# Optimization experiments

Measured on AMD Instinct MI355X. Metric: run time of the kernel, lower is better.

Reference implementation:

```python
import jax, jax.numpy as jnp
import numpy as np

TAU = 0.1
MASK_VAL = 1e9


def setup_inputs() -> dict:
    key = jax.random.key(0)
    ka, kb = jax.random.split(key)
    B, D = 4096, 512
    return {
        "view_a": jax.random.normal(ka, (B, D), dtype=jnp.float32),
        "view_b": jax.random.normal(kb, (B, D), dtype=jnp.float32),
    }


def _l2norm(x):
    return x / jnp.maximum(jnp.linalg.norm(x, axis=-1, keepdims=True), 1e-12)


def reference(view_a, view_b):
    a = _l2norm(view_a)
    b = _l2norm(view_b)
    B = a.shape[0]
    labels = jnp.arange(B)  # start_i = 0 (single device)
    mask = jnp.eye(B, dtype=a.dtype) * MASK_VAL

    logits_aa = a @ a.T / TAU - mask
    logits_bb = b @ b.T / TAU - mask
    logits_ab = a @ b.T / TAU
    logits_ba = b @ a.T / TAU

    full_a = jnp.concatenate([logits_ab, logits_aa], axis=1)  # [B, 2B]
    full_b = jnp.concatenate([logits_ba, logits_bb], axis=1)

    def ce(logits):
        logp = jax.nn.log_softmax(logits, axis=-1)
        return -jnp.mean(jnp.take_along_axis(logp, labels[:, None], axis=-1))

    loss = (ce(full_a) + ce(full_b)) / 2

    pred = jnp.argmax(full_a, axis=-1)
    acc = 100.0 * jnp.sum(pred == labels) / B
    return loss, acc
```

## Files before the change

kernel.cpp:

```cpp
#include <hip/hip_runtime.h>
#include <stdint.h>


#define BN 4096
#define DK 512
#define NSPLIT 16
#define NEG_BIG -1e30f
#define SCL 0.15625f
#define SCL2 0.225396744f
#define C2 14.4269504f
#define TILE_BYTES (64 * DK)

typedef __attribute__((ext_vector_type(16))) float floatx16;
typedef __attribute__((ext_vector_type(8))) int intx8;

__global__ void __launch_bounds__(256) prep_kernel(
    const float* __restrict__ A, const float* __restrict__ Bv,
    unsigned char* __restrict__ An, unsigned char* __restrict__ Bn,
    float* __restrict__ diag, float* __restrict__ out) {
  if (blockIdx.x == 0 && threadIdx.x < 2) out[threadIdx.x] = 0.0f;
  const int w = threadIdx.x >> 6, lane = threadIdx.x & 63;
  const int row = blockIdx.x * 4 + w;
  const float4* pa4 = (const float4*)(A + (size_t)row * DK);
  const float4* pb4 = (const float4*)(Bv + (size_t)row * DK);
  float4 a0 = pa4[lane * 2], a1 = pa4[lane * 2 + 1];
  float4 b0 = pb4[lane * 2], b1 = pb4[lane * 2 + 1];
  float ssa = a0.x * a0.x + a0.y * a0.y + a0.z * a0.z + a0.w * a0.w +
              a1.x * a1.x + a1.y * a1.y + a1.z * a1.z + a1.w * a1.w;
  float ssb = b0.x * b0.x + b0.y * b0.y + b0.z * b0.z + b0.w * b0.w +
              b1.x * b1.x + b1.y * b1.y + b1.z * b1.z + b1.w * b1.w;
  float sab = a0.x * b0.x + a0.y * b0.y + a0.z * b0.z + a0.w * b0.w +
              a1.x * b1.x + a1.y * b1.y + a1.z * b1.z + a1.w * b1.w;
#pragma unroll
  for (int off = 32; off > 0; off >>= 1) {
    ssa += __shfl_xor(ssa, off);
    ssb += __shfl_xor(ssb, off);
    sab += __shfl_xor(sab, off);
  }
  float na = fmaxf(sqrtf(ssa), 1e-12f);
  float nb = fmaxf(sqrtf(ssb), 1e-12f);
  const float s = 8.0f;
  float sa = s / na, sb = s / nb;
  const int doff = (lane >> 2) * 32 + (lane & 1) * 16 + ((lane >> 1) & 1) * 8;
  {
    int v0 = __builtin_amdgcn_cvt_pk_fp8_f32(a0.x * sa, a0.y * sa, 0, false);
    v0 = __builtin_amdgcn_cvt_pk_fp8_f32(a0.z * sa, a0.w * sa, v0, true);
    int v1 = __builtin_amdgcn_cvt_pk_fp8_f32(a1.x * sa, a1.y * sa, 0, false);
    v1 = __builtin_amdgcn_cvt_pk_fp8_f32(a1.z * sa, a1.w * sa, v1, true);
    int2 pv; pv.x = v0; pv.y = v1;
    *(int2*)(An + (size_t)row * DK + doff) = pv;
  }
  {
    int v0 = __builtin_amdgcn_cvt_pk_fp8_f32(b0.x * sb, b0.y * sb, 0, false);
    v0 = __builtin_amdgcn_cvt_pk_fp8_f32(b0.z * sb, b0.w * sb, v0, true);
    int v1 = __builtin_amdgcn_cvt_pk_fp8_f32(b1.x * sb, b1.y * sb, 0, false);
    v1 = __builtin_amdgcn_cvt_pk_fp8_f32(b1.z * sb, b1.w * sb, v1, true);
    int2 pv; pv.x = v0; pv.y = v1;
    *(int2*)(Bn + (size_t)row * DK + doff) = pv;
  }
  if (lane == 0) diag[row] = (sab / (na * nb)) * 10.0f;
}

__global__ void __launch_bounds__(256, 2) tiles_kernel(
    const unsigned char* __restrict__ An, const unsigned char* __restrict__ Bn,
    float* __restrict__ pSA, float* __restrict__ pMA, float* __restrict__ pSB) {
  __shared__ __align__(16) unsigned char smem[2 * TILE_BYTES];

  const int rb = blockIdx.x;
  const int split = blockIdx.y;
  const int tid = threadIdx.x;
  const int lane = tid & 63, w = tid >> 6;
  const int n5 = lane & 31, h = lane >> 5;
  const int r0 = rb * 128;
  const int myrow = r0 + w * 32 + n5;

  intx8 aw[8];
  auto loadfrags = [&](const unsigned char* base) {
    const unsigned char* p = base + (size_t)myrow * DK + h * 16;
#pragma unroll
    for (int i = 0; i < 8; ++i) {
      int4 c0 = *(const int4*)(p + i * 64);
      int4 c1 = *(const int4*)(p + i * 64 + 32);
      intx8 v = {c0.x, c0.y, c0.z, c0.w, c1.x, c1.y, c1.z, c1.w};
      aw[i] = v;
    }
  };

  float l[16], mx[16];
#pragma unroll
  for (int r = 0; r < 16; ++r) { l[r] = 0.f; mx[r] = NEG_BIG; }

  auto stage = [&](unsigned char* buf, int jt) {
    const unsigned char* csrc = (jt < 64) ? An : Bn;
    const int cb = (jt & 63) * 64;
#pragma unroll
    for (int ii = 0; ii < 8; ++ii) {
      const int cp = w * 8 + ii;
      const int cl = cp * 2 + h;
      const unsigned char* src =
          csrc + (size_t)(cb + cl) * DK + ((n5 ^ (cl & 31)) * 16);
      __builtin_amdgcn_global_load_lds(
          (const __attribute__((address_space(1))) void*)src,
          (__attribute__((address_space(3))) void*)(buf + cp * 1024),
          16, 0, 0);
    }
  };

  stage(smem, split * 8);
  loadfrags(An);
  __syncthreads();

  for (int u = 0; u < 16; ++u) {
    const int t = u & 7;
    const int jt = split * 8 + t;
    unsigned char* cur = smem + (u & 1) * TILE_BYTES;
    unsigned char* nxt = smem + ((u + 1) & 1) * TILE_BYTES;
    if (u < 15) stage(nxt, split * 8 + ((t + 1) & 7));

    floatx16 acc[2];
#pragma unroll
    for (int cs = 0; cs < 2; ++cs)
#pragma unroll
      for (int r = 0; r < 16; ++r) acc[cs][r] = 0.f;

    const unsigned char* bbase = cur + (size_t)n5 * DK;
#pragma unroll
    for (int i = 0; i < 8; ++i) {
      const int p1 = ((4 * i + h) ^ n5) * 16;
      const int p2 = ((4 * i + 2 + h) ^ n5) * 16;
#pragma unroll
      for (int cs = 0; cs < 2; ++cs) {
        int4 b0 = *(const int4*)(bbase + cs * 32 * DK + p1);
        int4 b1 = *(const int4*)(bbase + cs * 32 * DK + p2);
        intx8 bw = {b0.x, b0.y, b0.z, b0.w, b1.x, b1.y, b1.z, b1.w};
        acc[cs] = __builtin_amdgcn_mfma_scale_f32_32x32x64_f8f6f4(
            aw[i], bw, acc[cs], 0, 0, 0, 0x7F7F7F7F, 0, 0x7F7F7F7F);
      }
    }

    const bool dtile = (((jt & 63) >> 1) == rb);
    const int colbase = (jt & 63) * 64;
    const bool passA = (u < 8);
#pragma unroll
    for (int r = 0; r < 16; ++r) {
      float v0 = acc[0][r], v1 = acc[1][r];
      if (dtile) {
        const int rowg = r0 + w * 32 + (r & 3) + 8 * (r >> 2) + 4 * h;
        if (rowg == colbase + n5)      v0 = NEG_BIG;
        if (rowg == colbase + 32 + n5) v1 = NEG_BIG;
      }
      if (passA) mx[r] = fmaxf(mx[r], fmaxf(v0, v1));
      l[r] += exp2f(fmaf(v0, SCL2, -C2)) + exp2f(fmaf(v1, SCL2, -C2));
    }

    if (u == 7) {
#pragma unroll
      for (int off = 1; off < 32; off <<= 1)
#pragma unroll
        for (int r = 0; r < 16; ++r) {
          l[r] += __shfl_xor(l[r], off);
          mx[r] = fmaxf(mx[r], __shfl_xor(mx[r], off));
        }
      if (n5 == 0) {
#pragma unroll
        for (int r = 0; r < 16; ++r) {
          const int row = r0 + w * 32 + (r & 3) + 8 * (r >> 2) + 4 * h;
          pSA[split * BN + row] = l[r];
          pMA[split * BN + row] = mx[r] * SCL;
        }
      }
#pragma unroll
      for (int r = 0; r < 16; ++r) l[r] = 0.f;
      loadfrags(Bn);
    }
    __syncthreads();
  }

#pragma unroll
  for (int off = 1; off < 32; off <<= 1)
#pragma unroll
    for (int r = 0; r < 16; ++r) l[r] += __shfl_xor(l[r], off);
  if (n5 == 0) {
#pragma unroll
    for (int r = 0; r < 16; ++r) {
      const int row = r0 + w * 32 + (r & 3) + 8 * (r >> 2) + 4 * h;
      pSB[split * BN + row] = l[r];
    }
  }
}

__global__ void __launch_bounds__(256) finalize_kernel(
    const float* __restrict__ pSA, const float* __restrict__ pMA,
    const float* __restrict__ pSB, const float* __restrict__ diag,
    float* __restrict__ out) {
  const int row = blockIdx.x * 256 + threadIdx.x;
  float SA = 0.f, SB = 0.f, MA = NEG_BIG;
#pragma unroll
  for (int s = 0; s < NSPLIT; ++s) {
    SA += pSA[s * BN + row];
    SB += pSB[s * BN + row];
    MA = fmaxf(MA, pMA[s * BN + row]);
  }
  const float d = diag[row];
  const float eL = exp2f(fmaf(d, 1.44269504f, -C2));
  float lseA = 10.0f + logf(SA + eL);
  float lseB = 10.0f + logf(SB + eL);
  float lossi = (lseA - d) + (lseB - d);
  float corr = (d >= MA) ? 1.f : 0.f;
#pragma unroll
  for (int off = 32; off > 0; off >>= 1) {
    lossi += __shfl_xor(lossi, off);
    corr += __shfl_xor(corr, off);
  }
  __shared__ float sred[2][4];
  if ((threadIdx.x & 63) == 0) {
    int w = threadIdx.x >> 6;
    sred[0][w] = lossi; sred[1][w] = corr;
  }
  __syncthreads();
  if (threadIdx.x == 0) {
    float ls = sred[0][0] + sred[0][1] + sred[0][2] + sred[0][3];
    float cs = sred[1][0] + sred[1][1] + sred[1][2] + sred[1][3];
    atomicAdd(&out[0], ls * (1.0f / 8192.0f));
    atomicAdd(&out[1], cs * (100.0f / 4096.0f));
  }
}

extern "C" void kernel_launch(void* const* d_in, const int* in_sizes, int n_in,
                              void* d_out, int out_size, void* d_ws, size_t ws_size,
                              hipStream_t stream) {
  const float* A = (const float*)d_in[0];
  const float* Bv = (const float*)d_in[1];
  unsigned char* An = (unsigned char*)d_ws;
  unsigned char* Bn = An + (size_t)BN * DK;
  float* diag = (float*)(Bn + (size_t)BN * DK);
  float* pSA = diag + BN;
  float* pMA = pSA + NSPLIT * BN;
  float* pSB = pMA + NSPLIT * BN;
  float* out = (float*)d_out;

  prep_kernel<<<BN / 4, 256, 0, stream>>>(A, Bv, An, Bn, diag, out);
  tiles_kernel<<<dim3(32, 16), 256, 0, stream>>>(An, Bn, pSA, pMA, pSB);
  finalize_kernel<<<BN / 256, 256, 0, stream>>>(pSA, pMA, pSB, diag, out);
}
```

Baseline: 121.9 us.

## Exploit Gram matrix symmetry: compute upper-triangle tiles only with row and column partial sums

Stacks A and B into a single 8192-row fp8 matrix and computes only the upper-triangular 128x64 tiles of its Gram matrix, one tile per block across 4160 blocks. Each tile contributes both row and column exp-sums (and maxes for the argmax), so the matmul work is roughly halved compared with computing A·[A;B]^T and B·[B;A]^T separately. In exchange, partial buffers grow to hundreds of slices that prep has to zero-fill and finalize has to reduce serially. Blocks are also much shorter, each loading a fresh A fragment with no double buffering, which adds launch and load overhead and reduces latency hiding.

```diff
diff --git a/kernel.cpp b/kernel.cpp
--- a/kernel.cpp
+++ b/kernel.cpp
@@ -4,21 +4,28 @@
 
 #define BN 4096
 #define DK 512
-#define NSPLIT 16
 #define NEG_BIG -1e30f
 #define SCL 0.15625f
 #define SCL2 0.225396744f
 #define C2 14.4269504f
 #define TILE_BYTES (64 * DK)
+#define NBLK 4160
 
 typedef __attribute__((ext_vector_type(16))) float floatx16;
 typedef __attribute__((ext_vector_type(8))) int intx8;
 
 __global__ void __launch_bounds__(256) prep_kernel(
     const float* __restrict__ A, const float* __restrict__ Bv,
-    unsigned char* __restrict__ An, unsigned char* __restrict__ Bn,
-    float* __restrict__ diag, float* __restrict__ out) {
-  if (blockIdx.x == 0 && threadIdx.x < 2) out[threadIdx.x] = 0.0f;
+    unsigned char* __restrict__ Gn, float* __restrict__ diag,
+    float* __restrict__ out, float* __restrict__ zbase,
+    float* __restrict__ mbase) {
+  const int gtid = blockIdx.x * 256 + threadIdx.x;
+  if (gtid < 2) out[gtid] = 0.0f;
+  for (int idx = gtid; idx < (128 + 64) * 8192; idx += 1024 * 256)
+    zbase[idx] = 0.0f;
+  for (int idx = gtid; idx < (128 + 32) * 4096; idx += 1024 * 256)
+    mbase[idx] = NEG_BIG;
+
   const int w = threadIdx.x >> 6, lane = threadIdx.x & 63;
   const int row = blockIdx.x * 4 + w;
   const float4* pa4 = (const float4*)(A + (size_t)row * DK);
@@ -48,7 +55,7 @@
     int v1 = __builtin_amdgcn_cvt_pk_fp8_f32(a1.x * sa, a1.y * sa, 0, false);
     v1 = __builtin_amdgcn_cvt_pk_fp8_f32(a1.z * sa, a1.w * sa, v1, true);
     int2 pv; pv.x = v0; pv.y = v1;
-    *(int2*)(An + (size_t)row * DK + doff) = pv;
+    *(int2*)(Gn + (size_t)row * DK + doff) = pv;
   }
   {
     int v0 = __builtin_amdgcn_cvt_pk_fp8_f32(b0.x * sb, b0.y * sb, 0, false);
@@ -56,27 +63,30 @@
     int v1 = __builtin_amdgcn_cvt_pk_fp8_f32(b1.x * sb, b1.y * sb, 0, false);
     v1 = __builtin_amdgcn_cvt_pk_fp8_f32(b1.z * sb, b1.w * sb, v1, true);
     int2 pv; pv.x = v0; pv.y = v1;
-    *(int2*)(Bn + (size_t)row * DK + doff) = pv;
+    *(int2*)(Gn + (size_t)(BN + row) * DK + doff) = pv;
   }
   if (lane == 0) diag[row] = (sab / (na * nb)) * 10.0f;
 }
 
 __global__ void __launch_bounds__(256, 2) tiles_kernel(
-    const unsigned char* __restrict__ An, const unsigned char* __restrict__ Bn,
-    float* __restrict__ pSA, float* __restrict__ pMA, float* __restrict__ pSB) {
-  __shared__ __align__(16) unsigned char smem[2 * TILE_BYTES];
-
-  const int rb = blockIdx.x;
-  const int split = blockIdx.y;
+    const unsigned char* __restrict__ Gn,
+    float* __restrict__ pRS, float* __restrict__ pCS,
+    float* __restrict__ pRM, float* __restrict__ pCM) {
+  __shared__ __align__(16) unsigned char smem[TILE_BYTES / 2 + 2048];
+
+  int bid = blockIdx.x, I = 0;
+  while (bid >= 128 - 2 * I) { bid -= 128 - 2 * I; ++I; }
+  const int j = 2 * I + bid;
+
   const int tid = threadIdx.x;
   const int lane = tid & 63, w = tid >> 6;
   const int n5 = lane & 31, h = lane >> 5;
-  const int r0 = rb * 128;
-  const int myrow = r0 + w * 32 + n5;
+  const int rbase = I * 128 + w * 32;
+  const int cbase = j * 64;
 
   intx8 aw[8];
-  auto loadfrags = [&](const unsigned char* base) {
-    const unsigned char* p = base + (size_t)myrow * DK + h * 16;
+  {
+    const unsigned char* p = Gn + (size_t)(rbase + n5) * DK + h * 16;
 #pragma unroll
     for (int i = 0; i < 8; ++i) {
       int4 c0 = *(const int4*)(p + i * 64);
@@ -84,124 +94,132 @@
       intx8 v = {c0.x, c0.y, c0.z, c0.w, c1.x, c1.y, c1.z, c1.w};
       aw[i] = v;
     }
-  };
-
-  float l[16], mx[16];
-#pragma unroll
-  for (int r = 0; r < 16; ++r) { l[r] = 0.f; mx[r] = NEG_BIG; }
-
-  auto stage = [&](unsigned char* buf, int jt) {
-    const unsigned char* csrc = (jt < 64) ? An : Bn;
-    const int cb = (jt & 63) * 64;
+  }
+
+  {
 #pragma unroll
     for (int ii = 0; ii < 8; ++ii) {
       const int cp = w * 8 + ii;
       const int cl = cp * 2 + h;
       const unsigned char* src =
-          csrc + (size_t)(cb + cl) * DK + ((n5 ^ (cl & 31)) * 16);
+          Gn + (size_t)(cbase + cl) * DK + ((n5 ^ (cl & 31)) * 16);
       __builtin_amdgcn_global_load_lds(
           (const __attribute__((address_space(1))) void*)src,
-          (__attribute__((address_space(3))) void*)(buf + cp * 1024),
+          (__attribute__((address_space(3))) void*)(smem + cp * 1024),
           16, 0, 0);
     }
-  };
-
-  stage(smem, split * 8);
-  loadfrags(An);
+  }
   __syncthreads();
 
-  for (int u = 0; u < 16; ++u) {
-    const int t = u & 7;
-    const int jt = split * 8 + t;
-    unsigned char* cur = smem + (u & 1) * TILE_BYTES;
-    unsigned char* nxt = smem + ((u + 1) & 1) * TILE_BYTES;
-    if (u < 15) stage(nxt, split * 8 + ((t + 1) & 7));
-
-    floatx16 acc[2];
-#pragma unroll
-    for (int cs = 0; cs < 2; ++cs)
-#pragma unroll
-      for (int r = 0; r < 16; ++r) acc[cs][r] = 0.f;
-
-    const unsigned char* bbase = cur + (size_t)n5 * DK;
-#pragma unroll
-    for (int i = 0; i < 8; ++i) {
-      const int p1 = ((4 * i + h) ^ n5) * 16;
-      const int p2 = ((4 * i + 2 + h) ^ n5) * 16;
-#pragma unroll
-      for (int cs = 0; cs < 2; ++cs) {
-        int4 b0 = *(const int4*)(bbase + cs * 32 * DK + p1);
-        int4 b1 = *(const int4*)(bbase + cs * 32 * DK + p2);
-        intx8 bw = {b0.x, b0.y, b0.z, b0.w, b1.x, b1.y, b1.z, b1.w};
-        acc[cs] = __builtin_amdgcn_mfma_scale_f32_32x32x64_f8f6f4(
-            aw[i], bw, acc[cs], 0, 0, 0, 0x7F7F7F7F, 0, 0x7F7F7F7F);
-      }
-    }
-
-    const bool dtile = (((jt & 63) >> 1) == rb);
-    const int colbase = (jt & 63) * 64;
-    const bool passA = (u < 8);
+  floatx16 acc[2];
+#pragma unroll
+  for (int cs = 0; cs < 2; ++cs)
+#pragma unroll
+    for (int r = 0; r < 16; ++r) acc[cs][r] = 0.f;
+
+  const unsigned char* bbase = smem + (size_t)n5 * DK;
+#pragma unroll
+  for (int i = 0; i < 8; ++i) {
+    const int p1 = ((4 * i + h) ^ n5) * 16;
+    const int p2 = ((4 * i + 2 + h) ^ n5) * 16;
+#pragma unroll
+    for (int cs = 0; cs < 2; ++cs) {
+      int4 b0 = *(const int4*)(bbase + cs * 32 * DK + p1);
+      int4 b1 = *(const int4*)(bbase + cs * 32 * DK + p2);
+      intx8 bw = {b0.x, b0.y, b0.z, b0.w, b1.x, b1.y, b1.z, b1.w};
+      acc[cs] = __builtin_amdgcn_mfma_scale_f32_32x32x64_f8f6f4(
+          aw[i], bw, acc[cs], 0, 0, 0, 0x7F7F7F7F, 0, 0x7F7F7F7F);
+    }
+  }
+
+  const bool diagp = ((j >> 1) == I);
+  float l[16], mxr[16];
+  float csum0 = 0.f, csum1 = 0.f, cmax0 = NEG_BIG, cmax1 = NEG_BIG;
+#pragma unroll
+  for (int r = 0; r < 16; ++r) {
+    const int rowg = rbase + (r & 3) + 8 * (r >> 2) + 4 * h;
+    {
+      const int colg = cbase + n5;
+      const float v = acc[0][r];
+      const bool excl = (diagp && colg <= rowg) || (colg == rowg + BN);
+      const float e = excl ? 0.f : exp2f(fmaf(v, SCL2, -C2));
+      const float vm = excl ? NEG_BIG : v;
+      l[r] = e; mxr[r] = vm;
+      csum0 += e; cmax0 = fmaxf(cmax0, vm);
+    }
+    {
+      const int colg = cbase + 32 + n5;
+      const float v = acc[1][r];
+      const bool excl = (diagp && colg <= rowg) || (colg == rowg + BN);
+      const float e = excl ? 0.f : exp2f(fmaf(v, SCL2, -C2));
+      const float vm = excl ? NEG_BIG : v;
+      l[r] += e; mxr[r] = fmaxf(mxr[r], vm);
+      csum1 += e; cmax1 = fmaxf(cmax1, vm);
+    }
+  }
+
+#pragma unroll
+  for (int off = 1; off < 32; off <<= 1)
+#pragma unroll
+    for (int r = 0; r < 16; ++r) l[r] += __shfl_xor(l[r], off);
+  if (I < 32) {
+#pragma unroll
+    for (int off = 1; off < 32; off <<= 1)
+#pragma unroll
+      for (int r = 0; r < 16; ++r)
+        mxr[r] = fmaxf(mxr[r], __shfl_xor(mxr[r], off));
+  }
+  if (n5 == 0) {
 #pragma unroll
     for (int r = 0; r < 16; ++r) {
-      float v0 = acc[0][r], v1 = acc[1][r];
-      if (dtile) {
-        const int rowg = r0 + w * 32 + (r & 3) + 8 * (r >> 2) + 4 * h;
-        if (rowg == colbase + n5)      v0 = NEG_BIG;
-        if (rowg == colbase + 32 + n5) v1 = NEG_BIG;
-      }
-      if (passA) mx[r] = fmaxf(mx[r], fmaxf(v0, v1));
-      l[r] += exp2f(fmaf(v0, SCL2, -C2)) + exp2f(fmaf(v1, SCL2, -C2));
-    }
-
-    if (u == 7) {
-#pragma unroll
-      for (int off = 1; off < 32; off <<= 1)
-#pragma unroll
-        for (int r = 0; r < 16; ++r) {
-          l[r] += __shfl_xor(l[r], off);
-          mx[r] = fmaxf(mx[r], __shfl_xor(mx[r], off));
-        }
-      if (n5 == 0) {
-#pragma unroll
-        for (int r = 0; r < 16; ++r) {
-          const int row = r0 + w * 32 + (r & 3) + 8 * (r >> 2) + 4 * h;
-          pSA[split * BN + row] = l[r];
-          pMA[split * BN + row] = mx[r] * SCL;
-        }
-      }
-#pragma unroll
-      for (int r = 0; r < 16; ++r) l[r] = 0.f;
-      loadfrags(Bn);
-    }
-    __syncthreads();
-  }
-
-#pragma unroll
-  for (int off = 1; off < 32; off <<= 1)
-#pragma unroll
-    for (int r = 0; r < 16; ++r) l[r] += __shfl_xor(l[r], off);
-  if (n5 == 0) {
-#pragma unroll
-    for (int r = 0; r < 16; ++r) {
-      const int row = r0 + w * 32 + (r & 3) + 8 * (r >> 2) + 4 * h;
-      pSB[split * BN + row] = l[r];
+      const int rowg = rbase + (r & 3) + 8 * (r >> 2) + 4 * h;
+      pRS[(size_t)j * 8192 + rowg] = l[r];
+      if (I < 32) pRM[(size_t)j * 4096 + rowg] = mxr[r];
+    }
+  }
+
+  csum0 += __shfl_xor(csum0, 32);
+  csum1 += __shfl_xor(csum1, 32);
+  cmax0 = fmaxf(cmax0, __shfl_xor(cmax0, 32));
+  cmax1 = fmaxf(cmax1, __shfl_xor(cmax1, 32));
+  float* cps = (float*)(smem + TILE_BYTES / 2);
+  float* cpm = cps + 256;
+  if (h == 0) {
+    cps[w * 64 + n5] = csum0; cps[w * 64 + 32 + n5] = csum1;
+    cpm[w * 64 + n5] = cmax0; cpm[w * 64 + 32 + n5] = cmax1;
+  }
+  __syncthreads();
+  if (tid < 64) {
+    const float s =
+        cps[tid] + cps[64 + tid] + cps[128 + tid] + cps[192 + tid];
+    pCS[(size_t)I * 8192 + cbase + tid] = s;
+    if (j < 64) {
+      const float m = fmaxf(fmaxf(cpm[tid], cpm[64 + tid]),
+                            fmaxf(cpm[128 + tid], cpm[192 + tid]));
+      pCM[(size_t)I * 4096 + cbase + tid] = m;
     }
   }
 }
 
 __global__ void __launch_bounds__(256) finalize_kernel(
-    const float* __restrict__ pSA, const float* __restrict__ pMA,
-    const float* __restrict__ pSB, const float* __restrict__ diag,
-    float* __restrict__ out) {
-  const int row = blockIdx.x * 256 + threadIdx.x;
+    const float* __restrict__ pRS, const float* __restrict__ pCS,
+    const float* __restrict__ pRM, const float* __restrict__ pCM,
+    const float* __restrict__ diag, float* __restrict__ out) {
+  const int i = blockIdx.x * 256 + threadIdx.x;
   float SA = 0.f, SB = 0.f, MA = NEG_BIG;
-#pragma unroll
-  for (int s = 0; s < NSPLIT; ++s) {
-    SA += pSA[s * BN + row];
-    SB += pSB[s * BN + row];
-    MA = fmaxf(MA, pMA[s * BN + row]);
-  }
-  const float d = diag[row];
+  for (int s = 0; s < 128; ++s) {
+    SA += pRS[(size_t)s * 8192 + i];
+    SB += pRS[(size_t)s * 8192 + BN + i];
+  }
+  for (int s = 0; s < 64; ++s) {
+    SA += pCS[(size_t)s * 8192 + i];
+    SB += pCS[(size_t)s * 8192 + BN + i];
+  }
+  for (int s = 0; s < 128; ++s) MA = fmaxf(MA, pRM[(size_t)s * 4096 + i]);
+  for (int s = 0; s < 32; ++s)  MA = fmaxf(MA, pCM[(size_t)s * 4096 + i]);
+  MA *= SCL;
+
+  const float d = diag[i];
   const float eL = exp2f(fmaf(d, 1.44269504f, -C2));
   float lseA = 10.0f + logf(SA + eL);
   float lseB = 10.0f + logf(SB + eL);
@@ -231,15 +249,15 @@
                               hipStream_t stream) {
   const float* A = (const float*)d_in[0];
   const float* Bv = (const float*)d_in[1];
-  unsigned char* An = (unsigned char*)d_ws;
-  unsigned char* Bn = An + (size_t)BN * DK;
-  float* diag = (float*)(Bn + (size_t)BN * DK);
-  float* pSA = diag + BN;
-  float* pMA = pSA + NSPLIT * BN;
-  float* pSB = pMA + NSPLIT * BN;
+  unsigned char* Gn = (unsigned char*)d_ws;
+  float* diag = (float*)(Gn + (size_t)8192 * DK);
+  float* pRS = diag + BN;
+  float* pCS = pRS + 128 * 8192;
+  float* pRM = pCS + 64 * 8192;
+  float* pCM = pRM + 128 * 4096;
   float* out = (float*)d_out;
 
-  prep_kernel<<<BN / 4, 256, 0, stream>>>(A, Bv, An, Bn, diag, out);
-  tiles_kernel<<<dim3(32, 16), 256, 0, stream>>>(An, Bn, pSA, pMA, pSB);
-  finalize_kernel<<<BN / 256, 256, 0, stream>>>(pSA, pMA, pSB, diag, out);
-}
+  prep_kernel<<<BN / 4, 256, 0, stream>>>(A, Bv, Gn, diag, out, pRS, pRM);
+  tiles_kernel<<<NBLK, 256, 0, stream>>>(Gn, pRS, pCS, pRM, pCM);
+  finalize_kernel<<<BN / 256, 256, 0, stream>>>(pRS, pCS, pRM, pCM, diag, out);
+}
```

Result: slower. 157.2 us (+29.0%).
